# Performance work log

Measured on AMD Instinct MI355X. Metric: run time of the kernel, lower is better.

The kernel has to match this reference:

```python
import jax, jax.numpy as jnp
import numpy as np

B, N, DIN = 64, 4096, 256
S, D, MLP = 8, 256, 512
ITERS = 3
EPS = 1e-6
LN_EPS = 1e-5


def _ln(x, g, b):
    m = x.mean(-1, keepdims=True)
    v = ((x - m) ** 2).mean(-1, keepdims=True)
    return (x - m) * jax.lax.rsqrt(v + LN_EPS) * g + b


def setup_inputs() -> dict:
    key = jax.random.key(0)
    ks = jax.random.split(key, 12)
    sc = lambda fan: 1.0 / np.sqrt(fan)
    return {
        "inputs": jax.random.normal(ks[0], (B, N, DIN), jnp.float32),
        "slot_init": jax.random.normal(ks[1], (B, S, D), jnp.float32),
        "k_w": jax.random.normal(ks[2], (DIN, D), jnp.float32) * sc(DIN),
        "q_w": jax.random.normal(ks[3], (D, D), jnp.float32) * sc(D),
        "v_w": jax.random.normal(ks[4], (DIN, D), jnp.float32) * sc(DIN),
        "gru_wi": jax.random.normal(ks[5], (D, 3 * D), jnp.float32) * sc(D),
        "gru_wh": jax.random.normal(ks[6], (D, 3 * D), jnp.float32) * sc(D),
        "gru_bi": jnp.zeros((3 * D,), jnp.float32),
        "gru_bh": jnp.zeros((3 * D,), jnp.float32),
        "ln_in_g": jnp.ones((DIN,), jnp.float32),
        "ln_in_b": jnp.zeros((DIN,), jnp.float32),
        "ln_slots_g": jnp.ones((D,), jnp.float32),
        "ln_slots_b": jnp.zeros((D,), jnp.float32),
        "ln_ff_g": jnp.ones((D,), jnp.float32),
        "ln_ff_b": jnp.zeros((D,), jnp.float32),
        "mlp_w1": jax.random.normal(ks[7], (D, MLP), jnp.float32) * sc(D),
        "mlp_b1": jnp.zeros((MLP,), jnp.float32),
        "mlp_w2": jax.random.normal(ks[8], (MLP, D), jnp.float32) * sc(MLP),
        "mlp_b2": jnp.zeros((D,), jnp.float32),
    }


def _gru(x, h, wi, wh, bi, bh):
    gi = x @ wi + bi  # [*, 3D]
    gh = h @ wh + bh
    ir, iz, inn = jnp.split(gi, 3, axis=-1)
    hr, hz, hn = jnp.split(gh, 3, axis=-1)
    r = jax.nn.sigmoid(ir + hr)
    z = jax.nn.sigmoid(iz + hz)
    n = jnp.tanh(inn + r * hn)
    return (1.0 - z) * n + z * h


def reference(inputs, slot_init, k_w, q_w, v_w, gru_wi, gru_wh, gru_bi, gru_bh,
              ln_in_g, ln_in_b, ln_slots_g, ln_slots_b, ln_ff_g, ln_ff_b,
              mlp_w1, mlp_b1, mlp_w2, mlp_b2):
    x = _ln(inputs, ln_in_g, ln_in_b)            # [B,N,DIN]
    k = (x @ k_w) * (D ** -0.5)                  # [B,N,D]
    v = x @ v_w                                   # [B,N,D]
    slots = slot_init                             # [B,S,D]
    for _ in range(ITERS):
        prev = slots
        s = _ln(slots, ln_slots_g, ln_slots_b)
        q = s @ q_w                               # [B,S,D]
        dots = jnp.einsum('bid,bjd->bij', q, k)   # [B,S,N]
        attn = jax.nn.softmax(dots, axis=1) + EPS # softmax over slots!
        attn = attn / attn.sum(-1, keepdims=True) # renorm over tokens
        updates = jnp.einsum('bjd,bij->bid', v, attn)  # [B,S,D]
        slots = _gru(updates.reshape(-1, D), prev.reshape(-1, D),
                     gru_wi, gru_wh, gru_bi, gru_bh).reshape(B, S, D)
        h = _ln(slots, ln_ff_g, ln_ff_b)
        slots = slots + (jax.nn.relu(h @ mlp_w1 + mlp_b1) @ mlp_w2 + mlp_b2)
    return slots
```

## Files before the change

kernel.cpp:

```cpp
#include <hip/hip_runtime.h>
#include <cstdint>
#include <cstddef>


typedef __attribute__((ext_vector_type(8))) short short8;
typedef __attribute__((ext_vector_type(4))) float f32x4;
typedef __attribute__((ext_vector_type(4))) unsigned short us4;
typedef __attribute__((ext_vector_type(8))) unsigned short us8;

#define DEV static __device__ __forceinline__

DEV unsigned short f2bf(float f) {
  union { float f; unsigned int u; } v; v.f = f;
  unsigned int r = v.u + 0x7FFFu + ((v.u >> 16) & 1u);
  return (unsigned short)(r >> 16);
}

DEV f32x4 mfma16(short8 a, short8 b, f32x4 c) {
  return __builtin_amdgcn_mfma_f32_16x16x32_bf16(a, b, c, 0, 0, 0);
}

constexpr size_t O_KF   = 0;
constexpr size_t SZ_KF  = (size_t)64*256*8*64*8*2;
constexpr size_t O_VF   = O_KF + SZ_KF;
constexpr size_t SZ_VF  = (size_t)64*128*16*64*8*2;
constexpr size_t O_ACC  = O_VF + SZ_VF;
constexpr size_t SZ_ACC = (size_t)64*32*8*256*4;
constexpr size_t O_SUM  = O_ACC + SZ_ACC;
constexpr size_t SZ_SUM = (size_t)64*32*8*4;
constexpr size_t O_SL   = O_SUM + SZ_SUM;
constexpr size_t SZ_SL  = (size_t)64*8*256*4;
constexpr size_t O_QF   = O_SL + SZ_SL;
constexpr size_t SZ_QF  = (size_t)64*8*64*8*2;
constexpr size_t O_WKV  = O_QF + SZ_QF;
constexpr size_t SZ_WKV = (size_t)32*8*64*8*2;
constexpr size_t O_WQ   = O_WKV + SZ_WKV;
constexpr size_t SZ_WQ  = (size_t)16*8*64*8*2;
constexpr size_t O_WGRU = O_WQ + SZ_WQ;
constexpr size_t SZ_WGRU= (size_t)96*8*64*8*2;
constexpr size_t O_WM1  = O_WGRU + SZ_WGRU;
constexpr size_t SZ_WM1 = (size_t)32*8*64*8*2;
constexpr size_t O_WM2  = O_WM1 + SZ_WM1;
constexpr size_t SZ_WM2 = (size_t)16*16*64*8*2;
constexpr size_t WS_NEED= O_WM2 + SZ_WM2;

__global__ void prepack(
    const float* __restrict__ kw, const float* __restrict__ qw,
    const float* __restrict__ vw, const float* __restrict__ wi,
    const float* __restrict__ wh, const float* __restrict__ w1,
    const float* __restrict__ w2, const float* __restrict__ slot_init,
    unsigned short* __restrict__ wkv, unsigned short* __restrict__ wq_,
    unsigned short* __restrict__ wgru, unsigned short* __restrict__ wm1,
    unsigned short* __restrict__ wm2, float* __restrict__ slots)
{
  int idx = blockIdx.x * 256 + threadIdx.x;
  if (idx < 16384) {
    int ct = idx >> 9, dc = (idx >> 6) & 7, L = idx & 63;
    int col = ct*16 + (L & 15), k0 = dc*32 + ((L>>4)*8);
    if (col < 256) {
      for (int j = 0; j < 8; ++j) wkv[idx*8+j] = f2bf(kw[(size_t)(k0+j)*256 + col] * 0.0625f);
    } else {
      int c = col - 256;
      for (int j = 0; j < 8; ++j) wkv[idx*8+j] = f2bf(vw[(size_t)(k0+j)*256 + c]);
    }
  } else if (idx < 24576) {
    int t = idx - 16384;
    int ct = t >> 9, dc = (t >> 6) & 7, L = t & 63;
    int col = ct*16 + (L & 15), k0 = dc*32 + ((L>>4)*8);
    for (int j = 0; j < 8; ++j) wq_[t*8+j] = f2bf(qw[(size_t)(k0+j)*256 + col]);
  } else if (idx < 73728) {
    int t = idx - 24576;
    int ct = t >> 9, dc = (t >> 6) & 7, L = t & 63;
    int k0 = dc*32 + ((L>>4)*8);
    const float* W = (ct < 48) ? wi : wh;
    int col = ((ct < 48) ? ct : (ct - 48))*16 + (L & 15);
    for (int j = 0; j < 8; ++j) wgru[t*8+j] = f2bf(W[(size_t)(k0+j)*768 + col]);
  } else if (idx < 90112) {
    int t = idx - 73728;
    int ct = t >> 9, dc = (t >> 6) & 7, L = t & 63;
    int col = ct*16 + (L & 15), k0 = dc*32 + ((L>>4)*8);
    for (int j = 0; j < 8; ++j) wm1[t*8+j] = f2bf(w1[(size_t)(k0+j)*512 + col]);
  } else if (idx < 106496) {
    int t = idx - 90112;
    int ct = t >> 10, dc = (t >> 6) & 15, L = t & 63;
    int col = ct*16 + (L & 15), k0 = dc*32 + ((L>>4)*8);
    for (int j = 0; j < 8; ++j) wm2[t*8+j] = f2bf(w2[(size_t)(k0+j)*256 + col]);
  } else {
    int t = idx - 106496;
    f32x4 v = *(const f32x4*)(slot_init + (size_t)t*4);
    *(f32x4*)(slots + (size_t)t*4) = v;
  }
}

__global__ __launch_bounds__(512, 4) void gemm_kv(
    const float* __restrict__ x, const float* __restrict__ lng,
    const float* __restrict__ lnb, const unsigned short* __restrict__ wkv,
    unsigned short* __restrict__ kfr, unsigned short* __restrict__ vfr)
{
  __shared__ unsigned short smem[32768];
  int tid = threadIdx.x, w = tid >> 6, L = tid & 63;
  int m16 = L & 15, q = L >> 4;
  int blk = blockIdx.x;
  int b = blk >> 6;
  int n0 = (blk & 63) << 6;

  {
    int r = (w << 3) + (L & 7), t8 = L >> 3;
    const float* xr = x + ((size_t)((b << 12) + n0 + r) << 8) + (t8 << 5);
    float xv[32];
    float s = 0.f, s2 = 0.f;
#pragma unroll
    for (int i = 0; i < 8; ++i) {
      f32x4 v = *(const f32x4*)(xr + (i << 2));
#pragma unroll
      for (int jj = 0; jj < 4; ++jj) { float t = v[jj]; xv[i*4+jj] = t; s += t; s2 += t*t; }
    }
    s  += __shfl_xor(s, 8);  s  += __shfl_xor(s, 16);  s  += __shfl_xor(s, 32);
    s2 += __shfl_xor(s2, 8); s2 += __shfl_xor(s2, 16); s2 += __shfl_xor(s2, 32);
    float mean = s * 0.00390625f;
    float var  = s2 * 0.00390625f - mean * mean;
    float rstd = rsqrtf(fmaxf(var, 0.f) + 1e-5f);
    unsigned short* arow = smem + r * 264 + (t8 << 5);
    const float* gg = lng + (t8 << 5);
    const float* bb = lnb + (t8 << 5);
#pragma unroll
    for (int i = 0; i < 4; ++i) {
      f32x4 g0 = *(const f32x4*)(gg + (i << 3));
      f32x4 g1 = *(const f32x4*)(gg + (i << 3) + 4);
      f32x4 b0 = *(const f32x4*)(bb + (i << 3));
      f32x4 b1 = *(const f32x4*)(bb + (i << 3) + 4);
      us8 pk;
#pragma unroll
      for (int jj = 0; jj < 4; ++jj) {
        pk[jj]     = f2bf((xv[i*8+jj]   - mean) * rstd * g0[jj] + b0[jj]);
        pk[4 + jj] = f2bf((xv[i*8+4+jj] - mean) * rstd * g1[jj] + b1[jj]);
      }
      *(us8*)(arow + (i << 3)) = pk;
    }
  }
  __syncthreads();

  f32x4 acc[4][4];
#pragma unroll
  for (int mt = 0; mt < 4; ++mt)
#pragma unroll
    for (int c = 0; c < 4; ++c) acc[mt][c] = (f32x4){0.f,0.f,0.f,0.f};

#pragma unroll
  for (int dc = 0; dc < 8; ++dc) {
    short8 af[4];
#pragma unroll
    for (int mt = 0; mt < 4; ++mt)
      af[mt] = *(const short8*)(smem + ((mt << 4) + m16) * 264 + dc*32 + q*8);
#pragma unroll
    for (int c = 0; c < 4; ++c) {
      short8 bf = *(const short8*)(wkv + ((((w<<2)+c)*8 + dc)*64 + L) * 8);
#pragma unroll
      for (int mt = 0; mt < 4; ++mt)
        acc[mt][c] = mfma16(af[mt], bf, acc[mt][c]);
    }
  }
  __syncthreads();

  if (w < 4) {
#pragma unroll
    for (int mt = 0; mt < 4; ++mt)
#pragma unroll
      for (int c = 0; c < 4; ++c) {
        int col = (w << 6) + (c << 4) + m16;
        int dc = col >> 5, oct = (col >> 3) & 3, j = col & 7;
        int base = ((mt << 3) + dc)*64 + ((oct >> 1) << 5) + ((oct & 1) << 2) + q;
#pragma unroll
        for (int r = 0; r < 4; ++r)
          smem[(base + (r << 3))*8 + j] = f2bf(acc[mt][c][r]);
      }
  } else {
#pragma unroll
    for (int mt = 0; mt < 4; ++mt)
#pragma unroll
      for (int c = 0; c < 4; ++c) {
        int d = ((w - 4) << 6) + (c << 4) + m16;
        int dt = d >> 4;
        int tok = ((mt & 1) << 4) + (q << 2);
        int lp = m16 + ((tok >> 3) << 4), j0 = (q & 1) << 2;
        us4 pk;
#pragma unroll
        for (int r = 0; r < 4; ++r) pk[r] = f2bf(acc[mt][c][r]);
        *(us4*)&smem[16384 + ((mt >> 1) << 13) + ((dt << 6) + lp)*8 + j0] = pk;
      }
  }
  __syncthreads();
  {
    size_t kb = (size_t)b*256 + ((blk & 63) << 2);
#pragma unroll
    for (int ii = 0; ii < 4; ++ii) {
      int cix = ii*512 + tid;
      int rt = cix >> 9, dcs = (cix >> 6) & 7, p = cix & 63;
      short8 vv = *(const short8*)(smem + (size_t)cix*8);
      *(short8*)(kfr + (((kb + rt)*8 + dcs)*64 + p)*8) = vv;
    }
    size_t vb = (size_t)b*128 + ((blk & 63) << 1);
#pragma unroll
    for (int ii = 0; ii < 4; ++ii) {
      int cix = ii*512 + tid;
      int cc = cix >> 10, dt = (cix >> 6) & 15, lp = cix & 63;
      short8 vv = *(const short8*)(smem + 16384 + (size_t)cix*8);
      *(short8*)(vfr + (((vb + cc)*16 + dt)*64 + lp)*8) = vv;
    }
  }
}

__global__ __launch_bounds__(256, 3) void attn(
    const unsigned short* __restrict__ kfr,
    const unsigned short* __restrict__ vfr,
    const unsigned short* __restrict__ qfg,
    float* __restrict__ accp, float* __restrict__ sump)
{
  __shared__ float red[4][8][260];
  __shared__ float rsum[4][8];
  int tid = threadIdx.x, w = tid >> 6, L = tid & 63;
  int slot = L & 15, q = L >> 4;
  int bt = blockIdx.x, b = blockIdx.y;
  int wv = (bt << 2) + w;
  int pk = (L & 32) | ((L & 3) << 3) | ((L & 16) >> 2) | ((L >> 2) & 3);
  const unsigned short* kb = kfr + ((size_t)b << 20) + pk*8;
  const unsigned short* vbp = vfr + ((size_t)b << 20) + L*8;
  short8 qf[8];
#pragma unroll
  for (int dc = 0; dc < 8; ++dc)
    qf[dc] = *(const short8*)(qfg + ((size_t)b << 12) + (dc*64 + L)*8);
  f32x4 accU[16];
#pragma unroll
  for (int dt = 0; dt < 16; ++dt) accU[dt] = (f32x4){0.f,0.f,0.f,0.f};
  float rs = 0.f;

#pragma unroll
  for (int c = 0; c < 2; ++c) {
    int tb0 = (wv << 2) + (c << 1);
    int c32 = (wv << 1) + c;
    const unsigned short* kt = kb + (size_t)tb0 * 4096;
    const unsigned short* vt = vbp + (size_t)c32 * 8192;
    short8 vfA[8];
#pragma unroll
    for (int dt = 0; dt < 8; ++dt)
      vfA[dt] = *(const short8*)(vt + dt*512);
    f32x4 d0 = (f32x4){0.f,0.f,0.f,0.f}, d1 = (f32x4){0.f,0.f,0.f,0.f};
#pragma unroll
    for (int dc = 0; dc < 8; ++dc) {
      short8 k0 = *(const short8*)(kt + dc*512);
      short8 k1 = *(const short8*)(kt + 4096 + dc*512);
      d0 = mfma16(k0, qf[dc], d0);
      d1 = mfma16(k1, qf[dc], d1);
    }
    float p0[4], p1[4];
#pragma unroll
    for (int r = 0; r < 4; ++r) {
      float e = __expf(d0[r]);
      float ss = e;
      ss += __shfl_xor(ss, 1); ss += __shfl_xor(ss, 2); ss += __shfl_xor(ss, 4);
      float pv = (slot < 8) ? (e / ss + 1e-6f) : 0.f;
      rs += pv; p0[r] = pv;
    }
#pragma unroll
    for (int r = 0; r < 4; ++r) {
      float e = __expf(d1[r]);
      float ss = e;
      ss += __shfl_xor(ss, 1); ss += __shfl_xor(ss, 2); ss += __shfl_xor(ss, 4);
      float pv = (slot < 8) ? (e / ss + 1e-6f) : 0.f;
      rs += pv; p1[r] = pv;
    }
    short8 pb;
#pragma unroll
    for (int j = 0; j < 8; ++j) {
      int srcl = slot + ((q & 1) << 5) + ((j >> 2) << 4);
      float va = __shfl(p0[j & 3], srcl);
      float vb2 = __shfl(p1[j & 3], srcl);
      pb[j] = (short)f2bf((q >> 1) ? vb2 : va);
    }
#pragma unroll
    for (int dt = 0; dt < 8; ++dt) accU[dt] = mfma16(vfA[dt], pb, accU[dt]);
#pragma unroll
    for (int dt = 0; dt < 8; ++dt) {
      short8 vv = *(const short8*)(vt + (8 + dt)*512);
      accU[8 + dt] = mfma16(vv, pb, accU[8 + dt]);
    }
  }
  rs += __shfl_xor(rs, 16);
  rs += __shfl_xor(rs, 32);
  if (slot < 8) {
#pragma unroll
    for (int dt = 0; dt < 16; ++dt)
      *(f32x4*)&red[w][slot][dt*16 + (q << 2)] = accU[dt];
  }
  if (L < 8) rsum[w][L] = rs;
  __syncthreads();
  {
    int s = tid >> 5, dp = (tid & 31) << 3;
    f32x4 a0 = (f32x4){0.f,0.f,0.f,0.f}, a1 = (f32x4){0.f,0.f,0.f,0.f};
#pragma unroll
    for (int ww = 0; ww < 4; ++ww) {
      a0 += *(const f32x4*)&red[ww][s][dp];
      a1 += *(const f32x4*)&red[ww][s][dp + 4];
    }
    float* ab = accp + (((size_t)((b << 4) + bt)*8 + s) << 8) + dp;
    *(f32x4*)ab = a0;
    *(f32x4*)(ab + 4) = a1;
    if (tid < 8)
      sump[(((b << 4) + bt) << 3) + tid] =
          rsum[0][tid] + rsum[1][tid] + rsum[2][tid] + rsum[3][tid];
  }
}

DEV void ln_stats512(const float hpr[16][260], float stats[16][2], int tid) {
  int row = tid >> 5, seg = tid & 31;
  float s = 0.f, s2 = 0.f;
#pragma unroll
  for (int jj = 0; jj < 8; ++jj) { float v = hpr[row][seg*8 + jj]; s += v; s2 += v*v; }
  s  += __shfl_xor(s, 1);  s  += __shfl_xor(s, 2);  s  += __shfl_xor(s, 4);
  s  += __shfl_xor(s, 8);  s  += __shfl_xor(s, 16);
  s2 += __shfl_xor(s2, 1); s2 += __shfl_xor(s2, 2); s2 += __shfl_xor(s2, 4);
  s2 += __shfl_xor(s2, 8); s2 += __shfl_xor(s2, 16);
  if (seg == 0) {
    float mean = s * 0.00390625f;
    float var  = s2 * 0.00390625f - mean*mean;
    stats[row][0] = mean;
    stats[row][1] = rsqrtf(fmaxf(var, 0.f) + 1e-5f);
  }
}

__global__ __launch_bounds__(512, 2) void fuse(
    int mode, int last,
    float* __restrict__ slots,
    const float* __restrict__ accp, const float* __restrict__ sump,
    const unsigned short* __restrict__ wgru,
    const unsigned short* __restrict__ wm1,
    const unsigned short* __restrict__ wm2,
    const unsigned short* __restrict__ wq_,
    unsigned short* __restrict__ qfg,
    const float* __restrict__ gbi, const float* __restrict__ gbh,
    const float* __restrict__ lnsg, const float* __restrict__ lnsb,
    const float* __restrict__ lnfg, const float* __restrict__ lnfb,
    const float* __restrict__ mb1, const float* __restrict__ mb2,
    float* __restrict__ outp)
{
  __shared__ unsigned short uimg[4096];
  __shared__ unsigned short himg[4096];
  __shared__ unsigned short h1img[8192];
  __shared__ float hpr[16][260];
  __shared__ float stats[16][2];
  __shared__ float rowsum[8];
  int tid = threadIdx.x, w = tid >> 6, L = tid & 63;
  int m16 = L & 15, q = L >> 4;
  int b = blockIdx.x;
  for (int i = tid; i < 4096; i += 512) { uimg[i] = 0; himg[i] = 0; }
  __syncthreads();
  float hh[2][4];

  if (mode == 1) {
    if (tid < 8) {
      float s = 0.f;
      for (int p = 0; p < 16; ++p) s += sump[((b << 4) + p)*8 + tid];
      rowsum[tid] = s;
    }
    __syncthreads();
    {
      int s = tid >> 6, dp = (tid & 63) << 2;
      const float* base = accp + (((size_t)(b << 4)*8 + s) << 8) + dp;
      f32x4 a0 = (f32x4){0.f,0.f,0.f,0.f};
      for (int p = 0; p < 16; ++p)
        a0 += *(const f32x4*)(base + (size_t)p * 2048);
      float inv = 1.f / rowsum[s];
      int dc = dp >> 5, lp = s + ((dp >> 3) & 3)*16, j0 = dp & 7;
      us4 pk;
#pragma unroll
      for (int j = 0; j < 4; ++j) pk[j] = f2bf(a0[j]*inv);
      *(us4*)&uimg[(dc*64 + lp)*8 + j0] = pk;
      f32x4 h0 = *(const f32x4*)(slots + ((b << 3) + s)*256 + dp);
      us4 pk2;
#pragma unroll
      for (int j = 0; j < 4; ++j) pk2[j] = f2bf(h0[j]);
      *(us4*)&himg[(dc*64 + lp)*8 + j0] = pk2;
    }
    __syncthreads();
    f32x4 aI[2][3], aH[2][3];
#pragma unroll
    for (int i = 0; i < 2; ++i)
#pragma unroll
      for (int g = 0; g < 3; ++g) { aI[i][g] = (f32x4){0.f,0.f,0.f,0.f}; aH[i][g] = (f32x4){0.f,0.f,0.f,0.f}; }
#pragma unroll
    for (int dc = 0; dc < 8; ++dc) {
      short8 au = *(const short8*)(uimg + (dc*64 + L)*8);
      short8 ah = *(const short8*)(himg + (dc*64 + L)*8);
#pragma unroll
      for (int i = 0; i < 2; ++i) {
        int dt = (w << 1) + i;
#pragma unroll
        for (int g = 0; g < 3; ++g) {
          short8 bu = *(const short8*)(wgru + (((g*16 + dt)*8 + dc)*64 + L)*8);
          aI[i][g] = mfma16(au, bu, aI[i][g]);
          short8 bh = *(const short8*)(wgru + (((48 + g*16 + dt)*8 + dc)*64 + L)*8);
          aH[i][g] = mfma16(ah, bh, aH[i][g]);
        }
      }
    }
#pragma unroll
    for (int i = 0; i < 2; ++i) {
      int d = ((w << 1) + i)*16 + m16;
      float bir = gbi[d], biz = gbi[256+d], bin = gbi[512+d];
      float bhr = gbh[d], bhz = gbh[256+d], bhn = gbh[512+d];
#pragma unroll
      for (int r = 0; r < 4; ++r) {
        int s = (q << 2) + r;
        if (s < 8) {
          float ir = aI[i][0][r] + bir, iz = aI[i][1][r] + biz, in_ = aI[i][2][r] + bin;
          float hr = aH[i][0][r] + bhr, hz = aH[i][1][r] + bhz, hn = aH[i][2][r] + bhn;
          float rg = 1.f / (1.f + __expf(-(ir + hr)));
          float zg = 1.f / (1.f + __expf(-(iz + hz)));
          float nn = tanhf(in_ + rg * hn);
          float hv = slots[((b << 3) + s)*256 + d];
          float hp = (1.f - zg)*nn + zg*hv;
          hh[i][r] = hp;
          hpr[s][d] = hp;
        } else {
          hpr[s][d] = 0.f;
        }
      }
    }
    __syncthreads();
    ln_stats512(hpr, stats, tid);
    __syncthreads();
    {
      int s = tid >> 6, dp = (tid & 63) << 2;
      float mean = stats[s][0], rstd = stats[s][1];
      int dc = dp >> 5, lp = s + ((dp >> 3) & 3)*16, j0 = dp & 7;
      us4 pk;
#pragma unroll
      for (int j = 0; j < 4; ++j)
        pk[j] = f2bf((hpr[s][dp+j] - mean)*rstd*lnfg[dp+j] + lnfb[dp+j]);
      *(us4*)&uimg[(dc*64 + lp)*8 + j0] = pk;
    }
    __syncthreads();
    f32x4 a1[4];
#pragma unroll
    for (int c = 0; c < 4; ++c) a1[c] = (f32x4){0.f,0.f,0.f,0.f};
#pragma unroll
    for (int dc = 0; dc < 8; ++dc) {
      short8 aa = *(const short8*)(uimg + (dc*64 + L)*8);
#pragma unroll
      for (int c = 0; c < 4; ++c) {
        short8 bb = *(const short8*)(wm1 + ((((w<<2)+c)*8 + dc)*64 + L)*8);
        a1[c] = mfma16(aa, bb, a1[c]);
      }
    }
#pragma unroll
    for (int c = 0; c < 4; ++c) {
      int col = ((w << 2) + c)*16 + m16;
      float bv = mb1[col];
      int dc2 = col >> 5, lpb = ((col >> 3) & 3)*16, j = col & 7;
#pragma unroll
      for (int r = 0; r < 4; ++r) {
        int s = (q << 2) + r;
        float v = (s < 8) ? fmaxf(a1[c][r] + bv, 0.f) : 0.f;
        h1img[(dc2*64 + s + lpb)*8 + j] = f2bf(v);
      }
    }
    __syncthreads();
    f32x4 a2[2];
#pragma unroll
    for (int i = 0; i < 2; ++i) a2[i] = (f32x4){0.f,0.f,0.f,0.f};
#pragma unroll
    for (int dc2 = 0; dc2 < 16; ++dc2) {
      short8 aa = *(const short8*)(h1img + (dc2*64 + L)*8);
#pragma unroll
      for (int i = 0; i < 2; ++i) {
        short8 bb = *(const short8*)(wm2 + ((((w<<1)+i)*16 + dc2)*64 + L)*8);
        a2[i] = mfma16(aa, bb, a2[i]);
      }
    }
#pragma unroll
    for (int i = 0; i < 2; ++i) {
      int d = ((w << 1) + i)*16 + m16;
      float b2v = mb2[d];
#pragma unroll
      for (int r = 0; r < 4; ++r) {
        int s = (q << 2) + r;
        if (s < 8) {
          float o = a2[i][r] + b2v + hh[i][r];
          slots[((b << 3) + s)*256 + d] = o;
          if (last) outp[((b << 3) + s)*256 + d] = o;
          hpr[s][d] = o;
        }
      }
    }
    __syncthreads();
  } else {
    int s = tid >> 6, dp = (tid & 63) << 2;
#pragma unroll
    for (int j = 0; j < 4; ++j) {
      hpr[s][dp+j] = slots[((b << 3) + s)*256 + dp + j];
      hpr[8 + s][dp+j] = 0.f;
    }
    __syncthreads();
  }

  ln_stats512(hpr, stats, tid);
  __syncthreads();
  {
    int s = tid >> 6, dp = (tid & 63) << 2;
    float mean = stats[s][0], rstd = stats[s][1];
    int dc = dp >> 5, lp = s + ((dp >> 3) & 3)*16, j0 = dp & 7;
    us4 pk;
#pragma unroll
    for (int j = 0; j < 4; ++j)
      pk[j] = f2bf((hpr[s][dp+j] - mean)*rstd*lnsg[dp+j] + lnsb[dp+j]);
    *(us4*)&uimg[(dc*64 + lp)*8 + j0] = pk;
  }
  __syncthreads();
  {
    f32x4 aq[2];
#pragma unroll
    for (int i = 0; i < 2; ++i) aq[i] = (f32x4){0.f,0.f,0.f,0.f};
#pragma unroll
    for (int dc = 0; dc < 8; ++dc) {
      short8 aa = *(const short8*)(uimg + (dc*64 + L)*8);
#pragma unroll
      for (int i = 0; i < 2; ++i) {
        short8 bb = *(const short8*)(wq_ + ((((w<<1)+i)*8 + dc)*64 + L)*8);
        aq[i] = mfma16(aa, bb, aq[i]);
      }
    }
    unsigned short* qb = qfg + ((size_t)b << 12);
#pragma unroll
    for (int i = 0; i < 2; ++i) {
      int col = ((w << 1) + i)*16 + m16;
      int dc = col >> 5, lpb = ((col >> 3) & 3)*16, j = col & 7;
#pragma unroll
      for (int r = 0; r < 4; ++r) {
        int s = (q << 2) + r;
        qb[(dc*64 + s + lpb)*8 + j] = (s < 8) ? f2bf(aq[i][r]) : (unsigned short)0;
      }
    }
  }
}

extern "C" void kernel_launch(void* const* d_in, const int* in_sizes, int n_in,
                              void* d_out, int out_size, void* d_ws, size_t ws_size,
                              hipStream_t stream) {
  (void)in_sizes; (void)n_in; (void)out_size;
  if (ws_size < WS_NEED) return;

  const float* inputs    = (const float*)d_in[0];
  const float* slot_init = (const float*)d_in[1];
  const float* k_w       = (const float*)d_in[2];
  const float* q_w       = (const float*)d_in[3];
  const float* v_w       = (const float*)d_in[4];
  const float* gru_wi    = (const float*)d_in[5];
  const float* gru_wh    = (const float*)d_in[6];
  const float* gru_bi    = (const float*)d_in[7];
  const float* gru_bh    = (const float*)d_in[8];
  const float* ln_in_g   = (const float*)d_in[9];
  const float* ln_in_b   = (const float*)d_in[10];
  const float* ln_s_g    = (const float*)d_in[11];
  const float* ln_s_b    = (const float*)d_in[12];
  const float* ln_f_g    = (const float*)d_in[13];
  const float* ln_f_b    = (const float*)d_in[14];
  const float* m_w1      = (const float*)d_in[15];
  const float* m_b1      = (const float*)d_in[16];
  const float* m_w2      = (const float*)d_in[17];
  const float* m_b2      = (const float*)d_in[18];

  char* ws = (char*)d_ws;
  unsigned short* kfr  = (unsigned short*)(ws + O_KF);
  unsigned short* vfr  = (unsigned short*)(ws + O_VF);
  float*          accp = (float*)(ws + O_ACC);
  float*          sump = (float*)(ws + O_SUM);
  float*          slots= (float*)(ws + O_SL);
  unsigned short* qfg  = (unsigned short*)(ws + O_QF);
  unsigned short* wkv  = (unsigned short*)(ws + O_WKV);
  unsigned short* wq_  = (unsigned short*)(ws + O_WQ);
  unsigned short* wgru = (unsigned short*)(ws + O_WGRU);
  unsigned short* wm1  = (unsigned short*)(ws + O_WM1);
  unsigned short* wm2  = (unsigned short*)(ws + O_WM2);

  prepack<<<544, 256, 0, stream>>>(k_w, q_w, v_w, gru_wi, gru_wh, m_w1, m_w2,
                                   slot_init, wkv, wq_, wgru, wm1, wm2, slots);
  gemm_kv<<<4096, 512, 0, stream>>>(inputs, ln_in_g, ln_in_b, wkv, kfr, vfr);
  fuse<<<64, 512, 0, stream>>>(0, 0, slots, accp, sump, wgru, wm1, wm2, wq_, qfg,
                               gru_bi, gru_bh, ln_s_g, ln_s_b, ln_f_g, ln_f_b,
                               m_b1, m_b2, (float*)d_out);
  for (int it = 0; it < 3; ++it) {
    attn<<<dim3(16, 64), 256, 0, stream>>>(kfr, vfr, qfg, accp, sump);
    fuse<<<64, 512, 0, stream>>>(1, (it == 2) ? 1 : 0, slots, accp, sump, wgru,
                                 wm1, wm2, wq_, qfg, gru_bi, gru_bh, ln_s_g,
                                 ln_s_b, ln_f_g, ln_f_b, m_b1, m_b2,
                                 (float*)d_out);
  }
}
```

Measured before the change: 718.9 us.

## Split attention kernel over D halves to cut registers and raise occupancy

```diff
diff --git a/kernel.cpp b/kernel.cpp
--- a/kernel.cpp
+++ b/kernel.cpp
@@ -210,28 +210,34 @@
   }
 }
 
-__global__ __launch_bounds__(256, 3) void attn(
+__global__ __launch_bounds__(256, 5) void attn(
     const unsigned short* __restrict__ kfr,
     const unsigned short* __restrict__ vfr,
     const unsigned short* __restrict__ qfg,
     float* __restrict__ accp, float* __restrict__ sump)
 {
-  __shared__ float red[4][8][260];
+  __shared__ float red[4][8][132];
   __shared__ float rsum[4][8];
+  __shared__ unsigned short qlds[4096];
   int tid = threadIdx.x, w = tid >> 6, L = tid & 63;
   int slot = L & 15, q = L >> 4;
-  int bt = blockIdx.x, b = blockIdx.y;
+  int x = blockIdx.x, b = blockIdx.y;
+  int bt = x >> 1, half = x & 1;
   int wv = (bt << 2) + w;
   int pk = (L & 32) | ((L & 3) << 3) | ((L & 16) >> 2) | ((L >> 2) & 3);
   const unsigned short* kb = kfr + ((size_t)b << 20) + pk*8;
-  const unsigned short* vbp = vfr + ((size_t)b << 20) + L*8;
-  short8 qf[8];
-#pragma unroll
-  for (int dc = 0; dc < 8; ++dc)
-    qf[dc] = *(const short8*)(qfg + ((size_t)b << 12) + (dc*64 + L)*8);
-  f32x4 accU[16];
-#pragma unroll
-  for (int dt = 0; dt < 16; ++dt) accU[dt] = (f32x4){0.f,0.f,0.f,0.f};
+  const unsigned short* vbp = vfr + ((size_t)b << 20) + (half << 12) + L*8;
+
+  {
+    const unsigned short* qg = qfg + ((size_t)b << 12);
+    *(us8*)&qlds[tid*8]        = *(const us8*)(qg + tid*8);
+    *(us8*)&qlds[(tid+256)*8]  = *(const us8*)(qg + (tid+256)*8);
+  }
+  __syncthreads();
+
+  f32x4 accU[8];
+#pragma unroll
+  for (int dt = 0; dt < 8; ++dt) accU[dt] = (f32x4){0.f,0.f,0.f,0.f};
   float rs = 0.f;
 
 #pragma unroll
@@ -240,18 +246,21 @@
     int c32 = (wv << 1) + c;
     const unsigned short* kt = kb + (size_t)tb0 * 4096;
     const unsigned short* vt = vbp + (size_t)c32 * 8192;
-    short8 vfA[8];
-#pragma unroll
-    for (int dt = 0; dt < 8; ++dt)
+    short8 vfA[4];
+#pragma unroll
+    for (int dt = 0; dt < 4; ++dt)
       vfA[dt] = *(const short8*)(vt + dt*512);
     f32x4 d0 = (f32x4){0.f,0.f,0.f,0.f}, d1 = (f32x4){0.f,0.f,0.f,0.f};
+    __builtin_amdgcn_s_setprio(1);
 #pragma unroll
     for (int dc = 0; dc < 8; ++dc) {
       short8 k0 = *(const short8*)(kt + dc*512);
       short8 k1 = *(const short8*)(kt + 4096 + dc*512);
-      d0 = mfma16(k0, qf[dc], d0);
-      d1 = mfma16(k1, qf[dc], d1);
-    }
+      short8 qf = *(const short8*)(qlds + (dc*64 + L)*8);
+      d0 = mfma16(k0, qf, d0);
+      d1 = mfma16(k1, qf, d1);
+    }
+    __builtin_amdgcn_s_setprio(0);
     float p0[4], p1[4];
 #pragma unroll
     for (int r = 0; r < 4; ++r) {
@@ -277,35 +286,34 @@
       float vb2 = __shfl(p1[j & 3], srcl);
       pb[j] = (short)f2bf((q >> 1) ? vb2 : va);
     }
-#pragma unroll
-    for (int dt = 0; dt < 8; ++dt) accU[dt] = mfma16(vfA[dt], pb, accU[dt]);
-#pragma unroll
-    for (int dt = 0; dt < 8; ++dt) {
-      short8 vv = *(const short8*)(vt + (8 + dt)*512);
-      accU[8 + dt] = mfma16(vv, pb, accU[8 + dt]);
-    }
+    __builtin_amdgcn_s_setprio(1);
+#pragma unroll
+    for (int dt = 0; dt < 4; ++dt) accU[dt] = mfma16(vfA[dt], pb, accU[dt]);
+#pragma unroll
+    for (int dt = 4; dt < 8; ++dt) {
+      short8 vv = *(const short8*)(vt + dt*512);
+      accU[dt] = mfma16(vv, pb, accU[dt]);
+    }
+    __builtin_amdgcn_s_setprio(0);
   }
   rs += __shfl_xor(rs, 16);
   rs += __shfl_xor(rs, 32);
   if (slot < 8) {
 #pragma unroll
-    for (int dt = 0; dt < 16; ++dt)
+    for (int dt = 0; dt < 8; ++dt)
       *(f32x4*)&red[w][slot][dt*16 + (q << 2)] = accU[dt];
   }
   if (L < 8) rsum[w][L] = rs;
   __syncthreads();
   {
-    int s = tid >> 5, dp = (tid & 31) << 3;
-    f32x4 a0 = (f32x4){0.f,0.f,0.f,0.f}, a1 = (f32x4){0.f,0.f,0.f,0.f};
-#pragma unroll
-    for (int ww = 0; ww < 4; ++ww) {
+    int s = tid >> 5, dp = (tid & 31) << 2;
+    f32x4 a0 = (f32x4){0.f,0.f,0.f,0.f};
+#pragma unroll
+    for (int ww = 0; ww < 4; ++ww)
       a0 += *(const f32x4*)&red[ww][s][dp];
-      a1 += *(const f32x4*)&red[ww][s][dp + 4];
-    }
-    float* ab = accp + (((size_t)((b << 4) + bt)*8 + s) << 8) + dp;
+    float* ab = accp + (((size_t)(b << 5) + x)*8 + s)*128 + dp;
     *(f32x4*)ab = a0;
-    *(f32x4*)(ab + 4) = a1;
-    if (tid < 8)
+    if (half == 0 && tid < 8)
       sump[(((b << 4) + bt) << 3) + tid] =
           rsum[0][tid] + rsum[1][tid] + rsum[2][tid] + rsum[3][tid];
   }
@@ -365,7 +373,8 @@
     __syncthreads();
     {
       int s = tid >> 6, dp = (tid & 63) << 2;
-      const float* base = accp + (((size_t)(b << 4)*8 + s) << 8) + dp;
+      int hi = dp >> 7, dlo = dp & 127;
+      const float* base = accp + (((size_t)(b << 5) + hi)*8 + s)*128 + dlo;
       f32x4 a0 = (f32x4){0.f,0.f,0.f,0.f};
       for (int p = 0; p < 16; ++p)
         a0 += *(const f32x4*)(base + (size_t)p * 2048);
@@ -589,7 +598,7 @@
                                gru_bi, gru_bh, ln_s_g, ln_s_b, ln_f_g, ln_f_b,
                                m_b1, m_b2, (float*)d_out);
   for (int it = 0; it < 3; ++it) {
-    attn<<<dim3(16, 64), 256, 0, stream>>>(kfr, vfr, qfg, accp, sump);
+    attn<<<dim3(32, 64), 256, 0, stream>>>(kfr, vfr, qfg, accp, sump);
     fuse<<<64, 512, 0, stream>>>(1, (it == 2) ? 1 : 0, slots, accp, sump, wgru,
                                  wm1, wm2, wq_, qfg, gru_bi, gru_bh, ln_s_g,
                                  ln_s_b, ln_f_g, ln_f_b, m_b1, m_b2,
```

Result: slower. 903.1 us (+25.6%).
